# Performance work log

Measured on AMD Instinct MI355X. Metric: run time of the kernel, lower is better.

## Reference

```python
import jax, jax.numpy as jnp
import numpy as np

# Standard SMPL kinematic tree (parent of joint i); root parent = -1 (unused)
PARENTS = [-1, 0, 0, 0, 1, 2, 3, 4, 5, 6, 7, 8, 9, 9, 9, 12, 13, 14, 16, 17, 18, 19, 20, 21]
NUM_JOINTS = 24
NUM_VERTS = 6890
BATCH = 1024


def rodrigues(aa):
    """Axis-angle [..., 3] -> rotation matrices [..., 3, 3] (Rodrigues formula)."""
    eps = 1e-8
    theta = jnp.sqrt(jnp.sum(aa * aa, axis=-1, keepdims=True) + eps)  # [...,1]
    axis = aa / theta
    c = jnp.cos(theta)[..., None]
    s = jnp.sin(theta)[..., None]
    kx, ky, kz = axis[..., 0], axis[..., 1], axis[..., 2]
    zero = jnp.zeros_like(kx)
    K = jnp.stack([zero, -kz, ky, kz, zero, -kx, -ky, kx, zero], axis=-1)
    K = K.reshape(aa.shape[:-1] + (3, 3))
    I = jnp.eye(3, dtype=aa.dtype)
    return I + s * K + (1.0 - c) * (K @ K)


def make44(R, t):
    """R: [B,3,3], t: [B,3] -> homogeneous transform [B,4,4] (th_with_zeros)."""
    B = R.shape[0]
    top = jnp.concatenate([R, t[:, :, None]], axis=2)  # [B,3,4]
    bottom = jnp.broadcast_to(jnp.array([0.0, 0.0, 0.0, 1.0], dtype=R.dtype), (B, 1, 4))
    return jnp.concatenate([top, bottom], axis=1)


def setup_inputs() -> dict:
    key = jax.random.key(0)
    ks = jax.random.split(key, 8)
    return {
        "th_pose_axisang": jax.random.normal(ks[0], (BATCH, NUM_JOINTS * 3), dtype=jnp.float32),
        "th_betas": jax.random.normal(ks[1], (BATCH, 10), dtype=jnp.float32),
        "th_trans": jax.random.normal(ks[2], (BATCH, 3), dtype=jnp.float32),
        "v_template": jax.random.normal(ks[3], (NUM_VERTS, 3), dtype=jnp.float32),
        "shapedirs": jax.random.normal(ks[4], (NUM_VERTS, 3, 10), dtype=jnp.float32),
        "posedirs": jax.random.normal(ks[5], (NUM_VERTS, 3, 207), dtype=jnp.float32),
        "J_regressor": jax.random.uniform(ks[6], (NUM_JOINTS, NUM_VERTS), dtype=jnp.float32),
        "weights": jax.random.uniform(ks[7], (NUM_VERTS, NUM_JOINTS), dtype=jnp.float32),
    }


def reference(th_pose_axisang, th_betas, th_trans, v_template, shapedirs, posedirs, J_regressor, weights):
    B = th_pose_axisang.shape[0]
    dt = th_pose_axisang.dtype

    # pose map: all joint rotmats; non-root rotmats minus identity (subtract_flat_id)
    rots = rodrigues(th_pose_axisang.reshape(B, NUM_JOINTS, 3))  # [B,24,3,3]
    pose_map = (rots[:, 1:] - jnp.eye(3, dtype=dt)).reshape(B, (NUM_JOINTS - 1) * 9)  # [B,207]

    v_shaped = v_template[None] + jnp.einsum('vcs,bs->bvc', shapedirs, th_betas)   # [B,V,3]
    th_j = jnp.einsum('jv,bvc->bjc', J_regressor, v_shaped)                        # [B,24,3]
    v_posed = v_shaped + jnp.einsum('vcp,bp->bvc', posedirs, pose_map)             # [B,V,3]

    # forward kinematics along the fixed 24-joint chain
    results = [make44(rots[:, 0], th_j[:, 0])]
    for i in range(1, NUM_JOINTS):
        p = PARENTS[i]
        rel = make44(rots[:, i], th_j[:, i] - th_j[:, p])
        results.append(results[p] @ rel)
    G = jnp.stack(results, axis=1)  # [B,24,4,4] global transforms

    # remove rest-pose joint location from translation column (th_pack subtraction)
    j_h = jnp.concatenate([th_j, jnp.zeros((B, NUM_JOINTS, 1), dtype=dt)], axis=-1)  # [B,24,4]
    t_corr = jnp.einsum('bjmn,bjn->bjm', G, j_h)                                      # [B,24,4]
    G2 = jnp.concatenate([G[..., :3], (G[..., 3] - t_corr)[..., None]], axis=-1)      # [B,24,4,4]

    # linear blend skinning: per-vertex blended transform applied to rest shape
    T = jnp.einsum('bjmn,vj->bvmn', G2, weights)  # [B,V,4,4] (== th_T reordered)
    rest_h = jnp.concatenate([v_posed, jnp.ones((B, NUM_VERTS, 1), dtype=dt)], axis=-1)  # [B,V,4]
    th_verts = jnp.einsum('bvmn,bvn->bvm', T, rest_h)[..., :3]  # [B,V,3]

    th_jtr = G[:, :, :3, 3]  # [B,24,3]

    # th_trans is nonzero -> translation branch
    th_verts = th_verts + th_trans[:, None]
    th_jtr = th_jtr + th_trans[:, None]
    return th_verts, th_jtr
```

## Files before the change

kernel.cpp:

```cpp
#include <hip/hip_runtime.h>
#include <hip/hip_bf16.h>

#define NJ 24
#define NV 6890
#define NB 1024
#define V3 (NV*3)
#define JTR_OFF (NB*NV*3)

typedef __attribute__((ext_vector_type(8))) short bf16x8;
typedef __attribute__((ext_vector_type(4))) float f32x4;
typedef float f4u __attribute__((ext_vector_type(4), aligned(4)));

__constant__ int c_par[NJ] = {-1,0,0,0,1,2,3,4,5,6,7,8,9,9,9,12,13,14,16,17,18,19,20,21};

__global__ void kpre(const float* __restrict__ pdirs, const float* __restrict__ shdirs,
                     const float* __restrict__ vtempl, const float* __restrict__ wts,
                     const float* __restrict__ Jreg,
                     __hip_bfloat16* __restrict__ pdBsw, __hip_bfloat16* __restrict__ wtsB,
                     float* __restrict__ Jc)
{
    __shared__ float red[4][33];
    int bid = blockIdx.x;

    if (bid < 2268) {
        int cid = bid * 256 + threadIdx.x;
        int v64 = cid & 63;
        int t = cid >> 6;
        int kq = t & 3; t >>= 2;
        int c = t % 3; t /= 3;
        int kt = t % 7;
        int vt = t / 7;
        int v = vt * 64 + v64;
        int s = kt * 32 + kq * 8;

        ushort tmp[8] __attribute__((aligned(16)));
        if (v < NV && s + 8 <= 207) {
            const float* row = &pdirs[(v * 3 + c) * 207 + s];
            f4u lo = *(const f4u*)row;
            f4u hi = *(const f4u*)(row + 4);
#pragma unroll
            for (int j = 0; j < 4; ++j) {
                __hip_bfloat16 h0 = __float2bfloat16(lo[j]);
                __hip_bfloat16 h1 = __float2bfloat16(hi[j]);
                tmp[j]     = *(ushort*)&h0;
                tmp[j + 4] = *(ushort*)&h1;
            }
        } else if (v < NV && s == 208) {
            const float* sd = &shdirs[(v * 3 + c) * 10];
            f4u lo = *(const f4u*)(sd + 1);
            f4u hi = *(const f4u*)(sd + 5);
#pragma unroll
            for (int j = 0; j < 4; ++j) {
                __hip_bfloat16 h0 = __float2bfloat16(lo[j]);
                __hip_bfloat16 h1 = __float2bfloat16(hi[j]);
                tmp[j]     = *(ushort*)&h0;
                tmp[j + 4] = *(ushort*)&h1;
            }
        } else {
#pragma unroll
            for (int j = 0; j < 8; ++j) {
                int k = s + j;
                float val = 0.0f;
                if (v < NV) {
                    if (k < 207)       val = pdirs[(v * 3 + c) * 207 + k];
                    else if (k < 217)  val = shdirs[(v * 3 + c) * 10 + (k - 207)];
                    else if (k == 217) val = vtempl[v * 3 + c];
                }
                __hip_bfloat16 h = __float2bfloat16(val);
                tmp[j] = *(ushort*)&h;
            }
        }
        ((float4*)pdBsw)[cid] = *(const float4*)tmp;
    } else if (bid < 2376) {
        int t = (bid - 2268) * 256 + threadIdx.x;
        int v64 = t & 63;
        int kq = (t >> 6) & 3;
        int vt = t >> 8;
        int v = vt * 64 + v64;

        ushort tmp[8] __attribute__((aligned(16)));
#pragma unroll
        for (int j8 = 0; j8 < 8; ++j8) {
            int j = kq * 8 + j8;
            float val = (v < NV && j < NJ) ? wts[v * NJ + j] : 0.0f;
            __hip_bfloat16 h = __float2bfloat16(val);
            tmp[j8] = *(ushort*)&h;
        }
        ((float4*)wtsB)[t] = *(const float4*)tmp;
    } else {
        int rem = bid - 2376;
        int j = rem >> 2;
        int q = rem & 3;
        float acc[33];
#pragma unroll
        for (int i = 0; i < 33; ++i) acc[i] = 0.0f;

        for (int v = q * 256 + threadIdx.x; v < NV; v += 1024) {
            float r = Jreg[j * NV + v];
#pragma unroll
            for (int c = 0; c < 3; ++c) {
                acc[c * 11 + 10] += r * vtempl[v * 3 + c];
                const float* sd = &shdirs[(v * 3 + c) * 10];
#pragma unroll
                for (int s = 0; s < 10; ++s) acc[c * 11 + s] += r * sd[s];
            }
        }
#pragma unroll
        for (int i = 0; i < 33; ++i) {
            float x = acc[i];
            for (int o = 32; o > 0; o >>= 1) x += __shfl_down(x, o, 64);
            acc[i] = x;
        }
        int w = threadIdx.x >> 6, l = threadIdx.x & 63;
        if (l == 0) {
#pragma unroll
            for (int i = 0; i < 33; ++i) red[w][i] = acc[i];
        }
        __syncthreads();
        if (threadIdx.x < 33) {
            float s = red[0][threadIdx.x] + red[1][threadIdx.x] +
                      red[2][threadIdx.x] + red[3][threadIdx.x];
            atomicAdd(&Jc[j * 33 + threadIdx.x], s);
        }
    }
}

__device__ __forceinline__ void writeA(__hip_bfloat16* ABsw, int b, int k, float val)
{
    int btile = b >> 6, b6 = b & 63, kt = k >> 5, kq = (k >> 3) & 3, j = k & 7;
    __hip_bfloat16 h = __float2bfloat16(val);
    ABsw[((((btile * 7) + kt) * 4 + kq) * 64 + b6) * 8 + j] = h;
}

__global__ void k1(const float* __restrict__ pose, const float* __restrict__ betas,
                   const float* __restrict__ trans, const float* __restrict__ Jc,
                   __hip_bfloat16* __restrict__ ABsw, __hip_bfloat16* __restrict__ G2B,
                   float* __restrict__ out)
{
    __shared__ float rots[4][NJ][9];
    __shared__ float thj [4][NJ][3];
    __shared__ float res [4][NJ][16];

    int w = threadIdx.x >> 6;
    int l = threadIdx.x & 63;
    int b = blockIdx.x * 4 + w;

    if (l < NJ) {
        int j = l;
        float ax = pose[b * 72 + j * 3 + 0];
        float ay = pose[b * 72 + j * 3 + 1];
        float az = pose[b * 72 + j * 3 + 2];
        float theta = sqrtf(ax * ax + ay * ay + az * az + 1e-8f);
        float inv = 1.0f / theta;
        float kx = ax * inv, ky = ay * inv, kz = az * inv;
        float c = cosf(theta), s = sinf(theta), mc = 1.0f - c;
        float R[9];
        R[0] = 1.0f - mc * (ky * ky + kz * kz);
        R[1] = -s * kz + mc * (kx * ky);
        R[2] =  s * ky + mc * (kx * kz);
        R[3] =  s * kz + mc * (kx * ky);
        R[4] = 1.0f - mc * (kx * kx + kz * kz);
        R[5] = -s * kx + mc * (ky * kz);
        R[6] = -s * ky + mc * (kx * kz);
        R[7] =  s * kx + mc * (ky * kz);
        R[8] = 1.0f - mc * (kx * kx + ky * ky);
#pragma unroll
        for (int e = 0; e < 9; ++e) rots[w][j][e] = R[e];
        if (j >= 1) {
            int base = (j - 1) * 9;
#pragma unroll
            for (int e = 0; e < 9; ++e) {
                float val = R[e] - ((e == 0 || e == 4 || e == 8) ? 1.0f : 0.0f);
                writeA(ABsw, b, base + e, val);
            }
        }
#pragma unroll
        for (int c3 = 0; c3 < 3; ++c3) {
            float acc = Jc[(j * 3 + c3) * 11 + 10];
#pragma unroll
            for (int s10 = 0; s10 < 10; ++s10)
                acc += Jc[(j * 3 + c3) * 11 + s10] * betas[b * 10 + s10];
            thj[w][j][c3] = acc;
        }
    } else if (l < 41) {
        int k = 207 + (l - 24);
        float val;
        if (l < 34)       val = betas[b * 10 + (l - 24)];
        else if (l == 34) val = 1.0f;
        else              val = 0.0f;
        writeA(ABsw, b, k, val);
    }
    __syncthreads();

    if (l < 16) {
        int m = l >> 2, n = l & 3;
        float v;
        if (m < 3) v = (n < 3) ? rots[w][0][m * 3 + n] : thj[w][0][m];
        else       v = (n == 3) ? 1.0f : 0.0f;
        res[w][0][l] = v;
    }
    __syncthreads();
#pragma unroll
    for (int i = 1; i < NJ; ++i) {
        int p = c_par[i];
        if (l < 16) {
            int m = l >> 2, n = l & 3;
            float acc = 0.0f;
#pragma unroll
            for (int k3 = 0; k3 < 3; ++k3) {
                float relkn = (n < 3) ? rots[w][i][k3 * 3 + n]
                                      : (thj[w][i][k3] - thj[w][p][k3]);
                acc += res[w][p][m * 4 + k3] * relkn;
            }
            if (n == 3) acc += res[w][p][m * 4 + 3];
            res[w][i][l] = acc;
        }
        __syncthreads();
    }

    if (l < NJ) {
        int j = l;
#pragma unroll
        for (int c3 = 0; c3 < 3; ++c3)
            out[JTR_OFF + b * 72 + j * 3 + c3] = res[w][j][c3 * 4 + 3] + trans[b * 3 + c3];
    }
    for (int k = l; k < 384; k += 64) {
        int mc = k >> 5, j = k & 31;
        int m = mc >> 2, n = mc & 3;
        float v = 0.0f;
        if (j < NJ) {
            if (n < 3) v = res[w][j][m * 4 + n];
            else v = res[w][j][m * 4 + 3] - (res[w][j][m * 4 + 0] * thj[w][j][0] +
                                             res[w][j][m * 4 + 1] * thj[w][j][1] +
                                             res[w][j][m * 4 + 2] * thj[w][j][2]);
        }
        __hip_bfloat16 h = __float2bfloat16(v);
        G2B[mc * 32768 + ((((b >> 6) * 4) + (j >> 3)) * 64 + (b & 63)) * 8 + (j & 7)] = h;
    }
}

__device__ __forceinline__ void gld16(const void* g, void* l)
{
    __builtin_amdgcn_global_load_lds(
        (const __attribute__((address_space(1))) void*)g,
        (__attribute__((address_space(3))) void*)l, 16, 0, 0);
}

__launch_bounds__(256, 3)
__global__ void k2g(const __hip_bfloat16* __restrict__ pdBsw,
                    const __hip_bfloat16* __restrict__ ABsw,
                    const __hip_bfloat16* __restrict__ G2B,
                    const __hip_bfloat16* __restrict__ wtsB,
                    const float* __restrict__ trans,
                    float* __restrict__ outp)
{
    __shared__ __align__(16) char smem[2 * 16384];
    float* outs = (float*)smem;

    int tid = threadIdx.x;
    int wgid = blockIdx.y * 108 + blockIdx.x;
    int lin  = (wgid & 7) * 216 + (wgid >> 3);
    int vtile = lin >> 4;
    int btile = lin & 15;
    int wid = tid >> 6, lane = tid & 63;
    int waveb = wid & 1, wavev = wid >> 1;
    int kq = lane >> 4, l15 = lane & 15;

    auto stage = [&](int kb, int kt) {
        char* dst = smem + kb * 16384;
        const ushort* gA = (const ushort*)pdBsw + (size_t)(vtile * 7 + kt) * 6144;
        const ushort* gB = (const ushort*)ABsw  + (size_t)(btile * 7 + kt) * 2048;
#pragma unroll
        for (int i = 0; i < 3; ++i)
            gld16(gA + (i * 256 + wid * 64 + lane) * 8, dst + i * 4096 + wid * 1024);
        gld16(gB + (wid * 64 + lane) * 8, dst + 12288 + wid * 1024);
    };

    f32x4 acc[3][2][2] = {};

    int aoff = (kq * 64 + waveb * 32 + l15) * 8;
    int boff = (kq * 64 + wavev * 32 + l15) * 8;

    stage(0, 0);
    for (int kt = 0; kt < 7; ++kt) {
        if (kt < 6) {
            stage((kt + 1) & 1, kt + 1);
            asm volatile("s_waitcnt vmcnt(4)" ::: "memory");
        } else {
            asm volatile("s_waitcnt vmcnt(0)" ::: "memory");
        }
        __builtin_amdgcn_s_barrier();
        asm volatile("" ::: "memory");

        const ushort* As = (const ushort*)(smem + (kt & 1) * 16384);
        const ushort* Bs = As + 6144;

        bf16x8 af[2];
#pragma unroll
        for (int mi = 0; mi < 2; ++mi)
            af[mi] = *(const bf16x8*)&Bs[aoff + mi * 128];
#pragma unroll
        for (int c = 0; c < 3; ++c) {
            bf16x8 bfr[2];
#pragma unroll
            for (int ni = 0; ni < 2; ++ni)
                bfr[ni] = *(const bf16x8*)&As[boff + c * 2048 + ni * 128];
#pragma unroll
            for (int mi = 0; mi < 2; ++mi)
#pragma unroll
                for (int ni = 0; ni < 2; ++ni)
                    acc[c][mi][ni] = __builtin_amdgcn_mfma_f32_16x16x32_bf16(
                        af[mi], bfr[ni], acc[c][mi][ni], 0, 0, 0);
        }
        __builtin_amdgcn_s_barrier();
        asm volatile("" ::: "memory");
    }

    bf16x8 wf[2];
#pragma unroll
    for (int ni = 0; ni < 2; ++ni)
        wf[ni] = *(const bf16x8*)&wtsB[(((vtile * 4 + kq) * 64) +
                                        wavev * 32 + ni * 16 + l15) * 8];

    int bframe = ((btile * 4 + kq) * 64 + waveb * 32 + l15) * 8;

    float res3[2][2][4][3];
#pragma unroll
    for (int mi = 0; mi < 2; ++mi) {
#pragma unroll
        for (int m = 0; m < 3; ++m) {
            f32x4 T[4][2] = {};
#pragma unroll
            for (int c4 = 0; c4 < 4; ++c4) {
                int mc = m * 4 + c4;
                bf16x8 gf = *(const bf16x8*)&G2B[mc * 32768 + bframe + mi * 128];
#pragma unroll
                for (int ni = 0; ni < 2; ++ni)
                    T[c4][ni] = __builtin_amdgcn_mfma_f32_16x16x32_bf16(
                        gf, wf[ni], T[c4][ni], 0, 0, 0);
            }
#pragma unroll
            for (int ni = 0; ni < 2; ++ni) {
#pragma unroll
                for (int r = 0; r < 4; ++r) {
                    int bl = waveb * 32 + mi * 16 + (kq << 2) + r;
                    int b  = btile * 64 + bl;
                    float x = acc[0][mi][ni][r];
                    float y = acc[1][mi][ni][r];
                    float z = acc[2][mi][ni][r];
                    res3[mi][ni][r][m] = T[3][ni][r] + T[0][ni][r] * x +
                                         T[1][ni][r] * y + T[2][ni][r] * z +
                                         trans[b * 3 + m];
                }
            }
        }
    }

    int fvalid = (NV - vtile * 64) * 3;
    if (fvalid > 192) fvalid = 192;
#pragma unroll
    for (int pass = 0; pass < 2; ++pass) {
        if (waveb == pass) {
#pragma unroll
            for (int mi = 0; mi < 2; ++mi) {
#pragma unroll
                for (int ni = 0; ni < 2; ++ni) {
                    int vl = wavev * 32 + ni * 16 + l15;
#pragma unroll
                    for (int r = 0; r < 4; ++r) {
                        int row = mi * 16 + (kq << 2) + r;
#pragma unroll
                        for (int m = 0; m < 3; ++m)
                            outs[row * 204 + vl * 3 + m] = res3[mi][ni][r][m];
                    }
                }
            }
        }
        __syncthreads();
        if (lane < 48) {
            int fbase = lane * 4;
#pragma unroll
            for (int it = 0; it < 8; ++it) {
                int bl = wid * 8 + it;
                int b  = btile * 64 + pass * 32 + bl;
                const float* src = &outs[bl * 204 + fbase];
                float* dst = &outp[(size_t)b * V3 + (size_t)vtile * 192 + fbase];
                if (fbase + 4 <= fvalid) {
                    *(f4u*)dst = *(const f4u*)src;
                } else {
#pragma unroll
                    for (int k2 = 0; k2 < 4; ++k2)
                        if (fbase + k2 < fvalid) dst[k2] = src[k2];
                }
            }
        }
        if (pass == 0) __syncthreads();
    }
}

extern "C" void kernel_launch(void* const* d_in, const int* in_sizes, int n_in,
                              void* d_out, int out_size, void* d_ws, size_t ws_size,
                              hipStream_t stream)
{
    const float* pose   = (const float*)d_in[0];
    const float* betas  = (const float*)d_in[1];
    const float* trans  = (const float*)d_in[2];
    const float* vtempl = (const float*)d_in[3];
    const float* shdirs = (const float*)d_in[4];
    const float* pdirs  = (const float*)d_in[5];
    const float* Jreg   = (const float*)d_in[6];
    const float* wts    = (const float*)d_in[7];
    float* out = (float*)d_out;
    char* ws = (char*)d_ws;

    float* Jc              = (float*)(ws);
    __hip_bfloat16* ABsw   = (__hip_bfloat16*)(ws + 4096);
    __hip_bfloat16* G2B    = (__hip_bfloat16*)(ws + 462848);
    __hip_bfloat16* wtsB   = (__hip_bfloat16*)(ws + 1249280);
    __hip_bfloat16* pdBsw  = (__hip_bfloat16*)(ws + 1691648);

    hipMemsetAsync(Jc, 0, NJ * 33 * sizeof(float), stream);
    hipLaunchKernelGGL(kpre, dim3(2472), dim3(256), 0, stream,
                       pdirs, shdirs, vtempl, wts, Jreg, pdBsw, wtsB, Jc);
    hipLaunchKernelGGL(k1, dim3(NB / 4), dim3(256), 0, stream,
                       pose, betas, trans, Jc, ABsw, G2B, out);
    hipLaunchKernelGGL(k2g, dim3(108, 16), dim3(256), 0, stream,
                       pdBsw, ABsw, G2B, wtsB, trans, out);
}
```

Measured before the change: 176.4 us.

## Process two batch tiles per workgroup in k2g to reuse posedirs tile

Each k2g workgroup now handles two 64-row batch tiles instead of one, staging the shared posedirs A tile once and two activation B tiles per k-step. The grid is halved along the batch dimension, cutting redundant global/LDS loads of the posedirs slice and the per-block setup. In exchange it doubles accumulator registers and raises LDS use, which may lower occupancy under the 3-block launch bound, and it serialises the two epilogues per block.

```diff
diff --git a/kernel.cpp b/kernel.cpp
--- a/kernel.cpp
+++ b/kernel.cpp
@@ -254,29 +254,33 @@
                     const float* __restrict__ trans,
                     float* __restrict__ outp)
 {
-    __shared__ __align__(16) char smem[2 * 16384];
+    __shared__ __align__(16) char smem[2 * 20480];
     float* outs = (float*)smem;
 
     int tid = threadIdx.x;
     int wgid = blockIdx.y * 108 + blockIdx.x;
-    int lin  = (wgid & 7) * 216 + (wgid >> 3);
-    int vtile = lin >> 4;
-    int btile = lin & 15;
+    int lin  = (wgid & 7) * 108 + (wgid >> 3);
+    int vtile  = lin >> 3;
+    int btile2 = lin & 7;
     int wid = tid >> 6, lane = tid & 63;
     int waveb = wid & 1, wavev = wid >> 1;
     int kq = lane >> 4, l15 = lane & 15;
 
     auto stage = [&](int kb, int kt) {
-        char* dst = smem + kb * 16384;
+        char* dst = smem + kb * 20480;
         const ushort* gA = (const ushort*)pdBsw + (size_t)(vtile * 7 + kt) * 6144;
-        const ushort* gB = (const ushort*)ABsw  + (size_t)(btile * 7 + kt) * 2048;
 #pragma unroll
         for (int i = 0; i < 3; ++i)
             gld16(gA + (i * 256 + wid * 64 + lane) * 8, dst + i * 4096 + wid * 1024);
-        gld16(gB + (wid * 64 + lane) * 8, dst + 12288 + wid * 1024);
+#pragma unroll
+        for (int bt = 0; bt < 2; ++bt) {
+            const ushort* gB = (const ushort*)ABsw +
+                               (size_t)((btile2 * 2 + bt) * 7 + kt) * 2048;
+            gld16(gB + (wid * 64 + lane) * 8, dst + 12288 + bt * 4096 + wid * 1024);
+        }
     };
 
-    f32x4 acc[3][2][2] = {};
+    f32x4 acc[3][2][2][2] = {};
 
     int aoff = (kq * 64 + waveb * 32 + l15) * 8;
     int boff = (kq * 64 + wavev * 32 + l15) * 8;
@@ -285,20 +289,21 @@
     for (int kt = 0; kt < 7; ++kt) {
         if (kt < 6) {
             stage((kt + 1) & 1, kt + 1);
-            asm volatile("s_waitcnt vmcnt(4)" ::: "memory");
+            asm volatile("s_waitcnt vmcnt(5)" ::: "memory");
         } else {
             asm volatile("s_waitcnt vmcnt(0)" ::: "memory");
         }
         __builtin_amdgcn_s_barrier();
         asm volatile("" ::: "memory");
 
-        const ushort* As = (const ushort*)(smem + (kt & 1) * 16384);
-        const ushort* Bs = As + 6144;
-
-        bf16x8 af[2];
-#pragma unroll
-        for (int mi = 0; mi < 2; ++mi)
-            af[mi] = *(const bf16x8*)&Bs[aoff + mi * 128];
+        const ushort* As = (const ushort*)(smem + (kt & 1) * 20480);
+
+        bf16x8 af[2][2];
+#pragma unroll
+        for (int bt = 0; bt < 2; ++bt)
+#pragma unroll
+            for (int mi = 0; mi < 2; ++mi)
+                af[bt][mi] = *(const bf16x8*)&As[6144 + bt * 2048 + aoff + mi * 128];
 #pragma unroll
         for (int c = 0; c < 3; ++c) {
             bf16x8 bfr[2];
@@ -306,11 +311,13 @@
             for (int ni = 0; ni < 2; ++ni)
                 bfr[ni] = *(const bf16x8*)&As[boff + c * 2048 + ni * 128];
 #pragma unroll
-            for (int mi = 0; mi < 2; ++mi)
-#pragma unroll
-                for (int ni = 0; ni < 2; ++ni)
-                    acc[c][mi][ni] = __builtin_amdgcn_mfma_f32_16x16x32_bf16(
-                        af[mi], bfr[ni], acc[c][mi][ni], 0, 0, 0);
+            for (int bt = 0; bt < 2; ++bt)
+#pragma unroll
+                for (int mi = 0; mi < 2; ++mi)
+#pragma unroll
+                    for (int ni = 0; ni < 2; ++ni)
+                        acc[c][bt][mi][ni] = __builtin_amdgcn_mfma_f32_16x16x32_bf16(
+                            af[bt][mi], bfr[ni], acc[c][bt][mi][ni], 0, 0, 0);
         }
         __builtin_amdgcn_s_barrier();
         asm volatile("" ::: "memory");
@@ -322,79 +329,85 @@
         wf[ni] = *(const bf16x8*)&wtsB[(((vtile * 4 + kq) * 64) +
                                         wavev * 32 + ni * 16 + l15) * 8];
 
-    int bframe = ((btile * 4 + kq) * 64 + waveb * 32 + l15) * 8;
-
-    float res3[2][2][4][3];
-#pragma unroll
-    for (int mi = 0; mi < 2; ++mi) {
-#pragma unroll
-        for (int m = 0; m < 3; ++m) {
-            f32x4 T[4][2] = {};
-#pragma unroll
-            for (int c4 = 0; c4 < 4; ++c4) {
-                int mc = m * 4 + c4;
-                bf16x8 gf = *(const bf16x8*)&G2B[mc * 32768 + bframe + mi * 128];
-#pragma unroll
-                for (int ni = 0; ni < 2; ++ni)
-                    T[c4][ni] = __builtin_amdgcn_mfma_f32_16x16x32_bf16(
-                        gf, wf[ni], T[c4][ni], 0, 0, 0);
-            }
-#pragma unroll
-            for (int ni = 0; ni < 2; ++ni) {
-#pragma unroll
-                for (int r = 0; r < 4; ++r) {
-                    int bl = waveb * 32 + mi * 16 + (kq << 2) + r;
-                    int b  = btile * 64 + bl;
-                    float x = acc[0][mi][ni][r];
-                    float y = acc[1][mi][ni][r];
-                    float z = acc[2][mi][ni][r];
-                    res3[mi][ni][r][m] = T[3][ni][r] + T[0][ni][r] * x +
-                                         T[1][ni][r] * y + T[2][ni][r] * z +
-                                         trans[b * 3 + m];
-                }
-            }
-        }
-    }
-
     int fvalid = (NV - vtile * 64) * 3;
     if (fvalid > 192) fvalid = 192;
-#pragma unroll
-    for (int pass = 0; pass < 2; ++pass) {
-        if (waveb == pass) {
-#pragma unroll
-            for (int mi = 0; mi < 2; ++mi) {
+
+#pragma unroll
+    for (int bt = 0; bt < 2; ++bt) {
+        int btile = btile2 * 2 + bt;
+        int bframe = ((btile * 4 + kq) * 64 + waveb * 32 + l15) * 8;
+
+        float res3[2][2][4][3];
+#pragma unroll
+        for (int mi = 0; mi < 2; ++mi) {
+#pragma unroll
+            for (int m = 0; m < 3; ++m) {
+                f32x4 T[4][2] = {};
+#pragma unroll
+                for (int c4 = 0; c4 < 4; ++c4) {
+                    int mc = m * 4 + c4;
+                    bf16x8 gf = *(const bf16x8*)&G2B[mc * 32768 + bframe + mi * 128];
+#pragma unroll
+                    for (int ni = 0; ni < 2; ++ni)
+                        T[c4][ni] = __builtin_amdgcn_mfma_f32_16x16x32_bf16(
+                            gf, wf[ni], T[c4][ni], 0, 0, 0);
+                }
 #pragma unroll
                 for (int ni = 0; ni < 2; ++ni) {
-                    int vl = wavev * 32 + ni * 16 + l15;
 #pragma unroll
                     for (int r = 0; r < 4; ++r) {
-                        int row = mi * 16 + (kq << 2) + r;
-#pragma unroll
-                        for (int m = 0; m < 3; ++m)
-                            outs[row * 204 + vl * 3 + m] = res3[mi][ni][r][m];
+                        int bl = waveb * 32 + mi * 16 + (kq << 2) + r;
+                        int b  = btile * 64 + bl;
+                        float x = acc[0][bt][mi][ni][r];
+                        float y = acc[1][bt][mi][ni][r];
+                        float z = acc[2][bt][mi][ni][r];
+                        res3[mi][ni][r][m] = T[3][ni][r] + T[0][ni][r] * x +
+                                             T[1][ni][r] * y + T[2][ni][r] * z +
+                                             trans[b * 3 + m];
                     }
                 }
             }
         }
-        __syncthreads();
-        if (lane < 48) {
-            int fbase = lane * 4;
-#pragma unroll
-            for (int it = 0; it < 8; ++it) {
-                int bl = wid * 8 + it;
-                int b  = btile * 64 + pass * 32 + bl;
-                const float* src = &outs[bl * 204 + fbase];
-                float* dst = &outp[(size_t)b * V3 + (size_t)vtile * 192 + fbase];
-                if (fbase + 4 <= fvalid) {
-                    *(f4u*)dst = *(const f4u*)src;
-                } else {
-#pragma unroll
-                    for (int k2 = 0; k2 < 4; ++k2)
-                        if (fbase + k2 < fvalid) dst[k2] = src[k2];
+
+#pragma unroll
+        for (int pass = 0; pass < 2; ++pass) {
+            if (waveb == pass) {
+#pragma unroll
+                for (int mi = 0; mi < 2; ++mi) {
+#pragma unroll
+                    for (int ni = 0; ni < 2; ++ni) {
+                        int vl = wavev * 32 + ni * 16 + l15;
+#pragma unroll
+                        for (int r = 0; r < 4; ++r) {
+                            int row = mi * 16 + (kq << 2) + r;
+#pragma unroll
+                            for (int m = 0; m < 3; ++m)
+                                outs[row * 204 + vl * 3 + m] = res3[mi][ni][r][m];
+                        }
+                    }
                 }
             }
-        }
-        if (pass == 0) __syncthreads();
+            __syncthreads();
+            if (lane < 48) {
+                int fbase = lane * 4;
+#pragma unroll
+                for (int it = 0; it < 8; ++it) {
+                    int bl = wid * 8 + it;
+                    int b  = btile * 64 + pass * 32 + bl;
+                    const float* src = &outs[bl * 204 + fbase];
+                    float* dst = &outp[(size_t)b * V3 + (size_t)vtile * 192 + fbase];
+                    if (fbase + 4 <= fvalid) {
+                        *(f4u*)dst = *(const f4u*)src;
+                    } else {
+#pragma unroll
+                        for (int k2 = 0; k2 < 4; ++k2)
+                            if (fbase + k2 < fvalid) dst[k2] = src[k2];
+                    }
+                }
+            }
+            if (!(bt == 1 && pass == 1))
+                __syncthreads();
+        }
     }
 }
 
@@ -424,6 +437,6 @@
                        pdirs, shdirs, vtempl, wts, Jreg, pdBsw, wtsB, Jc);
     hipLaunchKernelGGL(k1, dim3(NB / 4), dim3(256), 0, stream,
                        pose, betas, trans, Jc, ABsw, G2B, out);
-    hipLaunchKernelGGL(k2g, dim3(108, 16), dim3(256), 0, stream,
+    hipLaunchKernelGGL(k2g, dim3(108, 8), dim3(256), 0, stream,
                        pdBsw, ABsw, G2B, wtsB, trans, out);
 }
```

New measurement: 192.8 us. +9.3%, slower.
